# Optimization experiments

Hardware: AMD Instinct MI355X
Metric: run time of the kernel (lower is better)

The kernel has to match this reference:

```python
import jax, jax.numpy as jnp
import numpy as np

T, B, DX, DA, H, Z, F = 256, 1024, 48, 16, 512, 32, 4
I = DX + DA


def setup_inputs() -> dict:
    key = jax.random.key(0)
    ks = jax.random.split(key, 20)
    s = 0.05
    inp = {
        "x": jax.random.normal(ks[0], (T, B, DX), dtype=jnp.float32),
        "a": jax.random.normal(ks[1], (T, B, DA), dtype=jnp.float32),
        "mask": (jax.random.uniform(ks[2], (T, B, DX)) < 0.8).astype(jnp.float32),
        # LSTM params (torch layout: [4H, I]/[4H, H], gate order i,f,g,o)
        "w_ih": jax.random.normal(ks[3], (4 * H, I), dtype=jnp.float32) * s,
        "w_hh": jax.random.normal(ks[4], (4 * H, H), dtype=jnp.float32) * s,
        "b_ih": jax.random.normal(ks[5], (4 * H,), dtype=jnp.float32) * s,
        "b_hh": jax.random.normal(ks[6], (4 * H,), dtype=jnp.float32) * s,
        # linear heads
        "lin_w": jax.random.normal(ks[7], (Z, H), dtype=jnp.float32) * s,
        "lin_b": jax.random.normal(ks[8], (Z,), dtype=jnp.float32) * s,
        "lv_w": jax.random.normal(ks[9], (Z, H), dtype=jnp.float32) * s,
        "lv_b": jax.random.normal(ks[10], (Z,), dtype=jnp.float32) * s,
        "u_w": jax.random.normal(ks[11], (F * Z, H), dtype=jnp.float32) * s,
        "u_b": jax.random.normal(ks[12], (F * Z,), dtype=jnp.float32) * s,
        "ww_w": jax.random.normal(ks[13], (F * Z, H), dtype=jnp.float32) * s,
        "ww_b": jax.random.normal(ks[14], (F * Z,), dtype=jnp.float32) * s,
        "bf_w": jax.random.normal(ks[15], (F, H), dtype=jnp.float32) * s,
        "bf_b": jax.random.normal(ks[16], (F,), dtype=jnp.float32) * s,
    }
    return inp


def _lstm_last_hidden(y, w_ih, w_hh, b_ih, b_hh):
    # y: [T, B, I] already time-reversed; returns h after the final step [B, H]
    def step(carry, xt):
        h, c = carry
        g = xt @ w_ih.T + h @ w_hh.T + (b_ih + b_hh)  # [B, 4H]
        gi, gf, gg, go = jnp.split(g, 4, axis=-1)
        c = jax.nn.sigmoid(gf) * c + jax.nn.sigmoid(gi) * jnp.tanh(gg)
        h = jax.nn.sigmoid(go) * jnp.tanh(c)
        return (h, c), None

    init = (jnp.zeros((y.shape[1], H), y.dtype), jnp.zeros((y.shape[1], H), y.dtype))
    (h, _), _ = jax.lax.scan(step, init, y)
    return h


def reference(x, a, mask, w_ih, w_hh, b_ih, b_hh, lin_w, lin_b, lv_w, lv_b,
              u_w, u_b, ww_w, ww_b, bf_w, bf_b):
    batch = x.shape[1]
    y_in = jnp.concatenate([x, a], axis=-1)                      # [T, B, I]
    mask_in = jnp.concatenate([mask, jnp.ones_like(a)], axis=-1)  # [T, B, I]
    y_rev = jnp.flip(y_in * mask_in, axis=0)                      # reversed-time loop
    out = _lstm_last_hidden(y_rev, w_ih, w_hh, b_ih, b_hh)        # [B, H] (== out[0] in torch)

    mu = out @ lin_w.T + lin_b
    log_var = out @ lv_w.T + lv_b
    # normalize=True branch
    mu = jnp.exp(mu) / 10.0
    log_var = log_var - 5.0

    u = (out @ u_w.T + u_b).reshape(batch, F, Z, 1)
    w = (out @ ww_w.T + ww_b).reshape(batch, F, 1, Z)
    b = (out @ bf_w.T + bf_b).reshape(batch, F, 1, 1)
    return mu, log_var, u, w, b
```

## Files before the change

kernel.cpp:

```cpp
#include <hip/hip_runtime.h>


typedef __attribute__((__ext_vector_type__(8))) short bx8;
typedef __attribute__((__ext_vector_type__(4))) float fx4;
typedef __attribute__((__ext_vector_type__(4))) unsigned ux4;
typedef unsigned long long u64;

#define NSTEP 256
#define NKT   18
#define ROWB  1184
#define GREG  18944
#define TRPO  37888

__device__ __forceinline__ short bf16_of(float f) {
  union { float f; unsigned u; } c; c.f = f;
  unsigned r = c.u + 0x7fffu + ((c.u >> 16) & 1u);
  return (short)(r >> 16);
}
__device__ __forceinline__ float fsigmoid(float x) {
  float e = __builtin_amdgcn_exp2f(-1.44269504f * x);
  return __builtin_amdgcn_rcpf(1.0f + e);
}
__device__ __forceinline__ float ftanh_(float x) {
  float e = __builtin_amdgcn_exp2f(2.88539008f * x);
  return 1.0f - 2.0f * __builtin_amdgcn_rcpf(1.0f + e);
}

__device__ __forceinline__ void poll_flags(const unsigned* p, unsigned tgt) {
  unsigned guard = 0;
  for (;;) {
    unsigned v;
    asm volatile("global_load_dword %0, %1, off sc0 sc1\n\ts_waitcnt vmcnt(0)"
                 : "=v"(v) : "v"(p) : "memory");
    if (__all((int)(v >= tgt))) break;
    if (++guard > (1u << 18)) break;
    __builtin_amdgcn_s_sleep(1);
  }
}

__global__ __launch_bounds__(256) void pack_y_kernel(
    const float* __restrict__ x, const float* __restrict__ a,
    const float* __restrict__ mk, short* __restrict__ y) {
  const int idx = blockIdx.x * 256 + threadIdx.x;
  const float* xp = x + (size_t)idx * 48;
  const float* mp = mk + (size_t)idx * 48;
  const float* ap = a + (size_t)idx * 16;
  short* yp = y + (size_t)idx * 64;
  float v[64];
#pragma unroll
  for (int j = 0; j < 12; ++j) {
    fx4 xv = *(const fx4*)(xp + j * 4);
    fx4 mv = *(const fx4*)(mp + j * 4);
#pragma unroll
    for (int t = 0; t < 4; ++t) v[j * 4 + t] = xv[t] * mv[t];
  }
#pragma unroll
  for (int j = 0; j < 4; ++j) {
    fx4 av = *(const fx4*)(ap + j * 4);
#pragma unroll
    for (int t = 0; t < 4; ++t) v[48 + j * 4 + t] = av[t];
  }
#pragma unroll
  for (int c = 0; c < 8; ++c) {
    bx8 o;
#pragma unroll
    for (int t = 0; t < 8; ++t) o[t] = bf16_of(v[c * 8 + t]);
    *(bx8*)(yp + c * 8) = o;
  }
}

__device__ __forceinline__ void do_half(
    int s, bool pub, bool pref,
    int gX, int gY, char* Ash, int regX, int regY, char* trpX,
    const bx8* Bf, const float* bias, float* cstX,
    const short* yslY, const char* hprevY, char* hnextX,
    float* __restrict__ hfinal, unsigned* flagX, const unsigned* pollY, unsigned tgtY,
    int tid, int wv, int l15, int l4, int srow, int sch,
    unsigned xsw, unsigned xm, int colh, int gn)
{
  fx4 acc[4];
#pragma unroll
  for (int nt = 0; nt < 4; ++nt) {
    fx4 z = {bias[nt], bias[nt], bias[nt], bias[nt]};
    acc[nt] = z;
  }
  const char* abase = Ash + regX + l15 * ROWB;
  const unsigned kbase = (unsigned)(l4 * 16);
#pragma unroll
  for (int kt = 0; kt < NKT; ++kt) {
    bx8 A0 = *(const bx8*)(abase + (int)(((unsigned)(kt * 64) + kbase) ^ xm));
#pragma unroll
    for (int nt = 0; nt < 4; ++nt)
      acc[nt] = __builtin_amdgcn_mfma_f32_16x16x32_bf16(A0, Bf[nt * NKT + kt], acc[nt], 0, 0, 0);
  }

  unsigned hs16[4];
#pragma unroll
  for (int r = 0; r < 4; ++r) {
    float gi = acc[0][r], gf = acc[1][r], gg = acc[2][r], go = acc[3][r];
    float c = fsigmoid(gf) * cstX[r] + fsigmoid(gi) * ftanh_(gg);
    cstX[r] = c;
    float h = fsigmoid(go) * ftanh_(c);
    hs16[r] = (unsigned)(unsigned short)bf16_of(h);
    if (!pub) hfinal[(size_t)(gX * 16 + l4 * 4 + r) * 512 + colh] = h;
  }

  if (pub) {
#pragma unroll
    for (int r = 0; r < 4; ++r)
      *(unsigned short*)(trpX + (l4 * 4 + r) * 128 + (wv * 16 + l15) * 2) =
          (unsigned short)hs16[r];
    asm volatile("s_waitcnt lgkmcnt(0)" ::: "memory");
    __builtin_amdgcn_sched_barrier(0);
  }

  if (pref) poll_flags(pollY, tgtY);

  ux4 vh0, vh1, vh2, vh3; u64 vy;
  if (pref) {
    const char* hq = hprevY + (size_t)(gY * 16 + srow) * 1024 + sch * 16;
    asm volatile("global_load_dwordx4 %0, %1, off sc0 sc1" : "=v"(vh0) : "v"(hq) : "memory");
    asm volatile("global_load_dwordx4 %0, %1, off offset:256 sc0 sc1" : "=v"(vh1) : "v"(hq) : "memory");
    asm volatile("global_load_dwordx4 %0, %1, off offset:512 sc0 sc1" : "=v"(vh2) : "v"(hq) : "memory");
    asm volatile("global_load_dwordx4 %0, %1, off offset:768 sc0 sc1" : "=v"(vh3) : "v"(hq) : "memory");
    const char* yp = (const char*)yslY + (size_t)(gY * 16 + srow) * 128 + sch * 8;
    asm volatile("global_load_dwordx2 %0, %1, off" : "=v"(vy) : "v"(yp) : "memory");
  }

  __builtin_amdgcn_s_barrier();

  if (pub) {
    u64 pv = *(const u64*)(trpX + srow * 128 + sch * 8);
    char* sb = hnextX + (size_t)(gX * 16 + srow) * 1024 + gn * 128 + sch * 8;
    asm volatile("global_store_dwordx2 %0, %1, off sc0 sc1" :: "v"(sb), "v"(pv) : "memory");
  }

  if (pref) {
    if (pub) asm volatile("s_waitcnt vmcnt(1)" ::: "memory");
    else     asm volatile("s_waitcnt vmcnt(0)" ::: "memory");
    __builtin_amdgcn_sched_barrier(0);
    char* lb = Ash + regY + srow * ROWB;
    *(ux4*)(lb + (int)(((unsigned)(sch * 16 + 0))   ^ xsw)) = vh0;
    *(ux4*)(lb + (int)(((unsigned)(sch * 16 + 256)) ^ xsw)) = vh1;
    *(ux4*)(lb + (int)(((unsigned)(sch * 16 + 512)) ^ xsw)) = vh2;
    *(ux4*)(lb + (int)(((unsigned)(sch * 16 + 768)) ^ xsw)) = vh3;
    *(u64*)(lb + (int)((1024u + sch * 8) ^ xsw)) = vy;
  }

  asm volatile("s_waitcnt vmcnt(0) lgkmcnt(0)" ::: "memory");
  __builtin_amdgcn_sched_barrier(0);
  __builtin_amdgcn_s_barrier();
  if (pub && tid == 0) {
    unsigned sv = (unsigned)(s + 1);
    asm volatile("global_store_dword %0, %1, off sc0 sc1" :: "v"(flagX), "v"(sv) : "memory");
  }
}

__global__ __launch_bounds__(256, 1) void lstm_rec(
    const short* __restrict__ yw,
    const float* __restrict__ w_hh,
    const float* __restrict__ w_ih,
    const float* __restrict__ b_ih, const float* __restrict__ b_hh,
    short* hbuf,
    float* __restrict__ hfinal,
    unsigned* ctr)
{
  __shared__ __align__(16) char Ash[82432];
  const int tid = threadIdx.x;
  const int wg  = blockIdx.x;
  const int xcd = wg & 7;
  const int ii  = wg >> 3;
  const int gn  = ii & 7;
  const int q   = ii >> 3;
  const int gA  = xcd * 4 + q;
  const int gB  = gA + 32;
  const int wv  = tid >> 6;
  const int lane = tid & 63;
  const int l15 = lane & 15;
  const int l4  = lane >> 4;

  bx8 Bf[4 * NKT];
  float bias[4];
  const int colh = gn * 64 + wv * 16 + l15;
#pragma unroll
  for (int nt = 0; nt < 4; ++nt) {
    const int col = nt * 512 + colh;
    bias[nt] = b_ih[col] + b_hh[col];
#pragma unroll
    for (int kt = 0; kt < NKT; ++kt) {
      const int k0 = kt * 32 + l4 * 8;
      const float* src = (k0 < 512) ? (w_hh + (size_t)col * 512 + k0)
                                    : (w_ih + (size_t)col * 64 + (k0 - 512));
      fx4 w0 = *(const fx4*)(src);
      fx4 w1 = *(const fx4*)(src + 4);
      bx8 b;
#pragma unroll
      for (int t = 0; t < 4; ++t) { b[t] = bf16_of(w0[t]); b[4 + t] = bf16_of(w1[t]); }
      Bf[nt * NKT + kt] = b;
    }
  }

  float cstA[4], cstB[4];
#pragma unroll
  for (int i = 0; i < 4; ++i) { cstA[i] = 0.f; cstB[i] = 0.f; }

  const int srow = tid >> 4;
  const int sch  = tid & 15;
  const unsigned xsw = (unsigned)((srow & 7) << 4);
  const unsigned xm  = (unsigned)((l15 & 7) << 4);
  char* trpA = Ash + TRPO;
  char* trpB = Ash + TRPO + 2048;

  unsigned* flbase = ctr + 1024;
  unsigned* flagA = flbase + (gA * 8 + gn) * 16;
  unsigned* flagB = flbase + (gB * 8 + gn) * 16;
  const unsigned* pollA = flbase + (gA * 8 + (lane & 7)) * 16;
  const unsigned* pollB = flbase + (gB * 8 + (lane & 7)) * 16;

  {
    u64 vy = *(const u64*)((const char*)(yw + (size_t)255 * 65536) +
                           (size_t)(gA * 16 + srow) * 128 + sch * 8);
    const u64* hq = (const u64*)((const char*)hbuf + (size_t)(gA * 16 + srow) * 1024) + sch * 2;
    char* lb = Ash + srow * ROWB;
#pragma unroll
    for (int j = 0; j < 4; ++j) {
      u64 a = hq[j * 32], b = hq[j * 32 + 1];
      *(u64*)(lb + (int)(((unsigned)(sch * 16 + j * 256))     ^ xsw)) = a;
      *(u64*)(lb + (int)(((unsigned)(sch * 16 + j * 256 + 8)) ^ xsw)) = b;
    }
    *(u64*)(lb + (int)((1024u + sch * 8) ^ xsw)) = vy;
    asm volatile("s_waitcnt lgkmcnt(0)" ::: "memory");
    __builtin_amdgcn_sched_barrier(0);
    __builtin_amdgcn_s_barrier();
  }

#pragma unroll 1
  for (int s = 0; s < NSTEP; ++s) {
    const char* hp = (const char*)hbuf + (size_t)(s & 1) * 1048576;
    char* hn = (char*)hbuf + (size_t)((s + 1) & 1) * 1048576;
    const short* ysl  = yw + (size_t)(255 - s) * 65536;
    const short* yslN = yw + (size_t)(s < 255 ? 254 - s : 0) * 65536;
    const bool pub = (s < 255);
    do_half(s, pub, true, gA, gB, Ash, 0, GREG, trpA, Bf, bias, cstA,
            ysl, hp, hn, hfinal, flagA, pollB, (unsigned)s,
            tid, wv, l15, l4, srow, sch, xsw, xm, colh, gn);
    do_half(s, pub, pub, gB, gA, Ash, GREG, 0, trpB, Bf, bias, cstB,
            yslN, hn, hn, hfinal, flagB, pollA, (unsigned)(s + 1),
            tid, wv, l15, l4, srow, sch, xsw, xm, colh, gn);
  }
}

__global__ __launch_bounds__(256) void heads_kernel(
    const float* __restrict__ hf,
    const float* __restrict__ lin_w, const float* __restrict__ lin_b,
    const float* __restrict__ lv_w,  const float* __restrict__ lv_b,
    const float* __restrict__ u_w,   const float* __restrict__ u_b,
    const float* __restrict__ ww_w,  const float* __restrict__ ww_b,
    const float* __restrict__ bf_w,  const float* __restrict__ bf_b,
    float* __restrict__ out)
{
  __shared__ float hs[64 * 513];
  const int tid = threadIdx.x;
  const int gb = blockIdx.x;
  const int cg = blockIdx.y;
  for (int i = tid; i < 8192; i += 256) {
    fx4 v = *(const fx4*)(hf + (size_t)gb * 32768 + (size_t)i * 4);
    const int row = i >> 7;
    const int k = (i * 4) & 511;
    float* d = hs + row * 513 + k;
    d[0] = v[0]; d[1] = v[1]; d[2] = v[2]; d[3] = v[3];
  }
  __syncthreads();
  const int r = tid & 63;
  const int cq = tid >> 6;
  const float* hrow = hs + r * 513;
  const int b_ = gb * 64 + r;
#pragma unroll 1
  for (int j = 0; j < 14; ++j) {
    const int cl = cq + 4 * j;
    if (cl >= 54) break;
    const int C = cg * 54 + cl;
    const float* wp; float bv;
    if (C < 32)       { wp = lin_w + (size_t)C * 512;        bv = lin_b[C]; }
    else if (C < 64)  { wp = lv_w + (size_t)(C - 32) * 512;  bv = lv_b[C - 32]; }
    else if (C < 192) { wp = u_w + (size_t)(C - 64) * 512;   bv = u_b[C - 64]; }
    else if (C < 320) { wp = ww_w + (size_t)(C - 192) * 512; bv = ww_b[C - 192]; }
    else              { wp = bf_w + (size_t)(C - 320) * 512; bv = bf_b[C - 320]; }
    float dot = 0.f;
#pragma unroll 8
    for (int k = 0; k < 512; k += 4) {
      fx4 w = *(const fx4*)(wp + k);
      dot += hrow[k] * w[0] + hrow[k + 1] * w[1] + hrow[k + 2] * w[2] + hrow[k + 3] * w[3];
    }
    const float res = bv + dot;
    if (C < 32)       out[(size_t)b_ * 32 + C] = __builtin_amdgcn_exp2f(res * 1.44269504f) * 0.1f;
    else if (C < 64)  out[32768 + (size_t)b_ * 32 + (C - 32)] = res - 5.f;
    else if (C < 192) out[65536 + (size_t)b_ * 128 + (C - 64)] = res;
    else if (C < 320) out[196608 + (size_t)b_ * 128 + (C - 192)] = res;
    else              out[327680 + (size_t)b_ * 4 + (C - 320)] = res;
  }
}

extern "C" void kernel_launch(void* const* d_in, const int* in_sizes, int n_in,
                              void* d_out, int out_size, void* d_ws, size_t ws_size,
                              hipStream_t stream) {
  (void)in_sizes; (void)n_in; (void)out_size; (void)ws_size;
  const float* x     = (const float*)d_in[0];
  const float* a     = (const float*)d_in[1];
  const float* mask  = (const float*)d_in[2];
  const float* w_ih  = (const float*)d_in[3];
  const float* w_hh  = (const float*)d_in[4];
  const float* b_ih  = (const float*)d_in[5];
  const float* b_hh  = (const float*)d_in[6];
  const float* lin_w = (const float*)d_in[7];
  const float* lin_b = (const float*)d_in[8];
  const float* lv_w  = (const float*)d_in[9];
  const float* lv_b  = (const float*)d_in[10];
  const float* u_w   = (const float*)d_in[11];
  const float* u_b   = (const float*)d_in[12];
  const float* ww_w  = (const float*)d_in[13];
  const float* ww_b  = (const float*)d_in[14];
  const float* bf_w  = (const float*)d_in[15];
  const float* bf_b  = (const float*)d_in[16];

  char* ws = (char*)d_ws;
  short* yw       = (short*)(ws);
  short* hbuf     = (short*)(ws + 33554432);
  float* hfinal   = (float*)(ws + 35651584);
  unsigned* ctr   = (unsigned*)(ws + 37748736);

  hipMemsetAsync(hbuf, 0, 2097152, stream);
  hipMemsetAsync(ctr, 0, 36864, stream);

  pack_y_kernel<<<1024, 256, 0, stream>>>(x, a, mask, yw);
  lstm_rec<<<256, 256, 0, stream>>>(yw, w_hh, w_ih, b_ih, b_hh, hbuf, hfinal, ctr);
  heads_kernel<<<dim3(16, 6), 256, 0, stream>>>(hfinal, lin_w, lin_b, lv_w, lv_b,
                                                u_w, u_b, ww_w, ww_b, bf_w, bf_b,
                                                (float*)d_out);
}
```

Baseline: 1.410 ms.

## Restructure LSTM inter-block flag protocol to single flag per group and earlier publish

Reworks the cross-workgroup synchronization in the persistent LSTM recurrence. Each workgroup now uses one flag with a monotonically increasing tag per half-step, and publishes it right after the local barrier, before polling peers. The y-slice load is hoisted to the start of each half so it overlaps the MFMA work. The sleep in the poll loop is removed and the spin guard is shortened, which lowers wake-up latency but costs more memory traffic while spinning. The flag is now stored before the h values are written to global memory, which risks a race unless the ordering is covered elsewhere.

After: 1.765 ms. 1.25x slower.

```diff
diff --git a/kernel.cpp b/kernel.cpp
--- a/kernel.cpp
+++ b/kernel.cpp
@@ -33,8 +33,7 @@
     asm volatile("global_load_dword %0, %1, off sc0 sc1\n\ts_waitcnt vmcnt(0)"
                  : "=v"(v) : "v"(p) : "memory");
     if (__all((int)(v >= tgt))) break;
-    if (++guard > (1u << 18)) break;
-    __builtin_amdgcn_s_sleep(1);
+    if (++guard > (1u << 16)) break;
   }
 }
 
@@ -70,14 +69,18 @@
 }
 
 __device__ __forceinline__ void do_half(
-    int s, bool pub, bool pref,
+    unsigned tag, bool pub, bool pref, bool fin,
     int gX, int gY, char* Ash, int regX, int regY, char* trpX,
     const bx8* Bf, const float* bias, float* cstX,
-    const short* yslY, const char* hprevY, char* hnextX,
-    float* __restrict__ hfinal, unsigned* flagX, const unsigned* pollY, unsigned tgtY,
+    const short* yslY, const char* hsrcY, char* hdstX,
+    float* __restrict__ hfinal, unsigned* myflag, const unsigned* pollp,
     int tid, int wv, int l15, int l4, int srow, int sch,
     unsigned xsw, unsigned xm, int colh, int gn)
 {
+  u64 vy = 0;
+  if (pref)
+    vy = *(const u64*)((const char*)yslY + (size_t)(gY * 16 + srow) * 128 + sch * 8);
+
   fx4 acc[4];
 #pragma unroll
   for (int nt = 0; nt < 4; ++nt) {
@@ -102,7 +105,7 @@
     cstX[r] = c;
     float h = fsigmoid(go) * ftanh_(c);
     hs16[r] = (unsigned)(unsigned short)bf16_of(h);
-    if (!pub) hfinal[(size_t)(gX * 16 + l4 * 4 + r) * 512 + colh] = h;
+    if (fin) hfinal[(size_t)(gX * 16 + l4 * 4 + r) * 512 + colh] = h;
   }
 
   if (pub) {
@@ -110,28 +113,32 @@
     for (int r = 0; r < 4; ++r)
       *(unsigned short*)(trpX + (l4 * 4 + r) * 128 + (wv * 16 + l15) * 2) =
           (unsigned short)hs16[r];
-    asm volatile("s_waitcnt lgkmcnt(0)" ::: "memory");
-    __builtin_amdgcn_sched_barrier(0);
-  }
-
-  if (pref) poll_flags(pollY, tgtY);
-
-  ux4 vh0, vh1, vh2, vh3; u64 vy;
+  }
+
+  if (!pub && !pref) return;
+
+  asm volatile("s_waitcnt vmcnt(0) lgkmcnt(0)" ::: "memory");
+  __builtin_amdgcn_sched_barrier(0);
+  __builtin_amdgcn_s_barrier();
+
+  if (tid == 0) {
+    unsigned sv = tag;
+    asm volatile("global_store_dword %0, %1, off sc0 sc1" :: "v"(myflag), "v"(sv) : "memory");
+  }
+
+  ux4 vh0, vh1, vh2, vh3;
   if (pref) {
-    const char* hq = hprevY + (size_t)(gY * 16 + srow) * 1024 + sch * 16;
+    poll_flags(pollp, tag);
+    const char* hq = hsrcY + (size_t)(gY * 16 + srow) * 1024 + sch * 16;
     asm volatile("global_load_dwordx4 %0, %1, off sc0 sc1" : "=v"(vh0) : "v"(hq) : "memory");
     asm volatile("global_load_dwordx4 %0, %1, off offset:256 sc0 sc1" : "=v"(vh1) : "v"(hq) : "memory");
     asm volatile("global_load_dwordx4 %0, %1, off offset:512 sc0 sc1" : "=v"(vh2) : "v"(hq) : "memory");
     asm volatile("global_load_dwordx4 %0, %1, off offset:768 sc0 sc1" : "=v"(vh3) : "v"(hq) : "memory");
-    const char* yp = (const char*)yslY + (size_t)(gY * 16 + srow) * 128 + sch * 8;
-    asm volatile("global_load_dwordx2 %0, %1, off" : "=v"(vy) : "v"(yp) : "memory");
-  }
-
-  __builtin_amdgcn_s_barrier();
+  }
 
   if (pub) {
     u64 pv = *(const u64*)(trpX + srow * 128 + sch * 8);
-    char* sb = hnextX + (size_t)(gX * 16 + srow) * 1024 + gn * 128 + sch * 8;
+    char* sb = hdstX + (size_t)(gX * 16 + srow) * 1024 + gn * 128 + sch * 8;
     asm volatile("global_store_dwordx2 %0, %1, off sc0 sc1" :: "v"(sb), "v"(pv) : "memory");
   }
 
@@ -147,13 +154,9 @@
     *(u64*)(lb + (int)((1024u + sch * 8) ^ xsw)) = vy;
   }
 
-  asm volatile("s_waitcnt vmcnt(0) lgkmcnt(0)" ::: "memory");
+  asm volatile("s_waitcnt lgkmcnt(0)" ::: "memory");
   __builtin_amdgcn_sched_barrier(0);
   __builtin_amdgcn_s_barrier();
-  if (pub && tid == 0) {
-    unsigned sv = (unsigned)(s + 1);
-    asm volatile("global_store_dword %0, %1, off sc0 sc1" :: "v"(flagX), "v"(sv) : "memory");
-  }
 }
 
 __global__ __launch_bounds__(256, 1) void lstm_rec(
@@ -212,10 +215,8 @@
   char* trpB = Ash + TRPO + 2048;
 
   unsigned* flbase = ctr + 1024;
-  unsigned* flagA = flbase + (gA * 8 + gn) * 16;
-  unsigned* flagB = flbase + (gB * 8 + gn) * 16;
-  const unsigned* pollA = flbase + (gA * 8 + (lane & 7)) * 16;
-  const unsigned* pollB = flbase + (gB * 8 + (lane & 7)) * 16;
+  unsigned* myflag = flbase + (gA * 8 + gn) * 16;
+  const unsigned* pollp = flbase + (gA * 8 + (lane & 7)) * 16;
 
   {
     u64 vy = *(const u64*)((const char*)(yw + (size_t)255 * 65536) +
@@ -236,16 +237,18 @@
 
 #pragma unroll 1
   for (int s = 0; s < NSTEP; ++s) {
-    const char* hp = (const char*)hbuf + (size_t)(s & 1) * 1048576;
-    char* hn = (char*)hbuf + (size_t)((s + 1) & 1) * 1048576;
-    const short* ysl  = yw + (size_t)(255 - s) * 65536;
-    const short* yslN = yw + (size_t)(s < 255 ? 254 - s : 0) * 65536;
-    const bool pub = (s < 255);
-    do_half(s, pub, true, gA, gB, Ash, 0, GREG, trpA, Bf, bias, cstA,
-            ysl, hp, hn, hfinal, flagA, pollB, (unsigned)s,
+    char* sl0 = (char*)hbuf + (size_t)(s & 1) * 1048576;
+    char* sl1 = (char*)hbuf + (size_t)((s + 1) & 1) * 1048576;
+    const short* ysB = yw + (size_t)(255 - s) * 65536;
+    const short* ysA = yw + (size_t)(s < 255 ? 254 - s : 0) * 65536;
+    const bool last = (s == NSTEP - 1);
+    do_half((unsigned)(2 * s), !last, true, last,
+            gA, gB, Ash, 0, GREG, trpA, Bf, bias, cstA,
+            ysB, sl0, sl1, hfinal, myflag, pollp,
             tid, wv, l15, l4, srow, sch, xsw, xm, colh, gn);
-    do_half(s, pub, pub, gB, gA, Ash, GREG, 0, trpB, Bf, bias, cstB,
-            yslN, hn, hn, hfinal, flagB, pollA, (unsigned)(s + 1),
+    do_half((unsigned)(2 * s + 1), !last, !last, last,
+            gB, gA, Ash, GREG, 0, trpB, Bf, bias, cstB,
+            ysA, sl1, sl1, hfinal, myflag, pollp,
             tid, wv, l15, l4, srow, sch, xsw, xm, colh, gn);
   }
 }
```
